# Optimization experiments

Measured on AMD Instinct MI355X. Metric: run time of the kernel, lower is better.

Reference implementation:

```python
import jax, jax.numpy as jnp
import numpy as np

B, S, H = 2, 1024, 1024
NH, NKV, HD = 16, 4, 64
E, TOPK, I = 8, 2, 3584
EPS = 1e-5
THETA = 1e6


def setup_inputs() -> dict:
    key = jax.random.key(0)
    ks = jax.random.split(key, 12)
    def w(k, shape, fan_in):
        return jax.random.normal(k, shape, dtype=jnp.float32) * (1.0 / np.sqrt(fan_in))
    return {
        "hidden_states": jax.random.normal(ks[0], (B, S, H), dtype=jnp.float32),
        "position_ids": jnp.broadcast_to(jnp.arange(S, dtype=jnp.int64)[None, :], (B, S)),
        "ln1_w": jnp.ones((H,), jnp.float32),
        "ln2_w": jnp.ones((H,), jnp.float32),
        "wq": w(ks[1], (H, NH * HD), H),
        "wk": w(ks[2], (H, NKV * HD), H),
        "wv": w(ks[3], (H, NKV * HD), H),
        "wo": w(ks[4], (NH * HD, H), NH * HD),
        "router_w": w(ks[5], (H, E), H),
        "w_gate": w(ks[6], (E, H, I), H),
        "w_up": w(ks[7], (E, H, I), H),
        "w_down": w(ks[8], (E, I, H), I),
    }


def _rmsnorm(x, w):
    xf = x.astype(jnp.float32)
    return (xf * jax.lax.rsqrt(jnp.mean(xf * xf, -1, keepdims=True) + EPS)).astype(x.dtype) * w


def _rope(x, pos):
    # x: [B,S,nh,HD], pos: [B,S]
    inv_freq = 1.0 / (THETA ** (jnp.arange(0, HD, 2, dtype=jnp.float32) / HD))
    ang = pos.astype(jnp.float32)[..., None] * inv_freq            # [B,S,HD/2]
    emb = jnp.concatenate([ang, ang], axis=-1)                      # [B,S,HD]
    cos, sin = jnp.cos(emb)[:, :, None, :], jnp.sin(emb)[:, :, None, :]
    x1, x2 = x[..., : HD // 2], x[..., HD // 2:]
    rot = jnp.concatenate([-x2, x1], axis=-1)
    return x * cos + rot * sin


def _forward(hidden_states, position_ids, ln1_w, ln2_w, wq, wk, wv, wo,
             router_w, w_gate, w_up, w_down):
    residual = hidden_states
    x = _rmsnorm(hidden_states, ln1_w)

    # ---- attention (GQA, causal, RoPE) ----
    q = (x @ wq).reshape(B, S, NH, HD)
    k = (x @ wk).reshape(B, S, NKV, HD)
    v = (x @ wv).reshape(B, S, NKV, HD)
    q = _rope(q, position_ids)
    k = _rope(k, position_ids)
    rep = NH // NKV
    k = jnp.repeat(k, rep, axis=2)  # [B,S,NH,HD]
    v = jnp.repeat(v, rep, axis=2)
    scores = jnp.einsum("bqhd,bkhd->bhqk", q, k) / np.sqrt(HD)
    causal = jnp.tril(jnp.ones((S, S), bool))
    scores = jnp.where(causal[None, None], scores, jnp.finfo(scores.dtype).min)
    probs = jax.nn.softmax(scores, axis=-1)
    attn = jnp.einsum("bhqk,bkhd->bqhd", probs, v).reshape(B, S, NH * HD)
    hidden = residual + attn @ wo

    # ---- MoE MLP ----
    residual = hidden
    xn = _rmsnorm(hidden, ln2_w).reshape(-1, H)               # [T,H]
    T = xn.shape[0]
    logits = xn @ router_w                                    # [T,E]
    rprobs = jax.nn.softmax(logits.astype(jnp.float32), axis=-1)
    topv, topi = jax.lax.top_k(rprobs, TOPK)                  # [T,TOPK]
    topv = topv / jnp.sum(topv, axis=-1, keepdims=True)       # normalize_top_k_affinities
    weights = jnp.zeros((T, E), jnp.float32).at[jnp.arange(T)[:, None], topi].set(topv)
    g = jnp.einsum("th,ehi->eti", xn, w_gate)                 # [E,T,I]
    u = jnp.einsum("th,ehi->eti", xn, w_up)
    a = jax.nn.silu(g) * u
    eo = jnp.einsum("eti,eih->eth", a, w_down)                # [E,T,H]
    moe = jnp.einsum("eth,te->th", eo, weights).reshape(B, S, H)
    return residual + moe


def reference(hidden_states, position_ids, ln1_w, ln2_w, wq, wk, wv, wo,
              router_w, w_gate, w_up, w_down):
    return _forward(hidden_states, position_ids, ln1_w, ln2_w, wq, wk, wv, wo,
                    router_w, w_gate, w_up, w_down)
```

## Files before the change

kernel.cpp:

```cpp
#include <hip/hip_runtime.h>
#include <hip/hip_bf16.h>
#include <math.h>

#define Bc 2
#define Sc 1024
#define Hc 1024
#define NHc 16
#define NKVc 4
#define HDc 64
#define Ec 8
#define TOPKc 2
#define Ic 3584
#define Tc (Bc*Sc)
#define EPSc 1e-5f

typedef __attribute__((ext_vector_type(8))) short bf16x8;
typedef __attribute__((ext_vector_type(4))) float f32x4;

__device__ __forceinline__ unsigned short f2bf(float f) {
    union { float f; unsigned u; } v; v.f = f;
    unsigned r = v.u + 0x7fffu + ((v.u >> 16) & 1u);
    return (unsigned short)(r >> 16);
}

__device__ __forceinline__ unsigned cvt_pk_bf16(float lo, float hi) {
    unsigned r;
    asm("v_cvt_pk_bf16_f32 %0, %1, %2" : "=v"(r) : "v"(lo), "v"(hi));
    return r;
}

static const size_t OFF_XN1  = 0;
static const size_t OFF_QB   = 8*1024*1024;
static const size_t OFF_KB   = OFF_QB + 8*1024*1024;
static const size_t OFF_VB   = OFF_KB + 2*1024*1024;
static const size_t OFF_XN2F = OFF_VB + 2*1024*1024;
static const size_t OFF_XN2B = OFF_XN2F + 8*1024*1024;
static const size_t OFF_ACT  = OFF_XN2B + 4*1024*1024;
static const size_t OFF_ROUTE= OFF_ACT + (size_t)4096*3584*2;

__global__ __launch_bounds__(256) void rmsnorm_kernel(const float* __restrict__ x,
        const float* __restrict__ w, float* __restrict__ outf,
        unsigned short* __restrict__ outb) {
    int t = blockIdx.x;
    int tid = threadIdx.x;
    const float* row = x + (size_t)t * Hc;
    float ss = 0.f;
    for (int h = tid; h < Hc; h += 256) { float v = row[h]; ss += v*v; }
    __shared__ float red[256];
    red[tid] = ss; __syncthreads();
    for (int s = 128; s > 0; s >>= 1) { if (tid < s) red[tid] += red[tid+s]; __syncthreads(); }
    float scale = rsqrtf(red[0] / (float)Hc + EPSc);
    for (int h = tid; h < Hc; h += 256) {
        float v = row[h] * scale * w[h];
        outf[(size_t)t*Hc + h] = v;
        if (outb) outb[(size_t)t*Hc + h] = f2bf(v);
    }
}

__global__ __launch_bounds__(256) void qkv_gemm(const float* __restrict__ A,
        const float* __restrict__ wq, const float* __restrict__ wk, const float* __restrict__ wv,
        float* __restrict__ qout, float* __restrict__ kout, float* __restrict__ vout) {
    __shared__ float As[64][17];
    __shared__ float Bs[16][65];
    int n0 = blockIdx.x * 64;
    int m0 = blockIdx.y * 64;
    int tid = threadIdx.x;
    int tx = tid & 15, ty = tid >> 4;
    const float* Bp; int ldb, c0;
    if (n0 < 1024)      { Bp = wq; ldb = 1024; c0 = n0; }
    else if (n0 < 1280) { Bp = wk; ldb = 256;  c0 = n0 - 1024; }
    else                { Bp = wv; ldb = 256;  c0 = n0 - 1280; }
    float acc[4][4] = {};
    for (int k0 = 0; k0 < 1024; k0 += 16) {
        #pragma unroll
        for (int i = 0; i < 4; i++) {
            int lin = tid + i*256; int r = lin >> 4, k = lin & 15;
            As[r][k] = A[(size_t)(m0 + r)*Hc + k0 + k];
        }
        #pragma unroll
        for (int i = 0; i < 4; i++) {
            int lin = tid + i*256; int r = lin >> 6, c = lin & 63;
            Bs[r][c] = Bp[(size_t)(k0 + r)*ldb + c0 + c];
        }
        __syncthreads();
        #pragma unroll
        for (int kk = 0; kk < 16; kk++) {
            float a[4], b[4];
            #pragma unroll
            for (int i = 0; i < 4; i++) a[i] = As[ty*4+i][kk];
            #pragma unroll
            for (int j = 0; j < 4; j++) b[j] = Bs[kk][tx*4+j];
            #pragma unroll
            for (int i = 0; i < 4; i++)
                #pragma unroll
                for (int j = 0; j < 4; j++) acc[i][j] += a[i]*b[j];
        }
        __syncthreads();
    }
    #pragma unroll
    for (int i = 0; i < 4; i++) {
        int m = m0 + ty*4 + i;
        #pragma unroll
        for (int j = 0; j < 4; j++) {
            int n = n0 + tx*4 + j;
            float val = acc[i][j];
            if (n < 1024)      qout[(size_t)m*1024 + n] = val;
            else if (n < 1280) kout[(size_t)m*256 + (n-1024)] = val;
            else               vout[(size_t)m*256 + (n-1280)] = val;
        }
    }
}

__global__ __launch_bounds__(256) void rope_kernel(float* __restrict__ q, float* __restrict__ k) {
    int idx = blockIdx.x*256 + threadIdx.x;
    const int total = Tc*(NHc+NKVc)*32;
    if (idx >= total) return;
    int d = idx & 31;
    int rest = idx >> 5;
    int head = rest % (NHc+NKVc);
    int t = rest / (NHc+NKVc);
    int s = t & (Sc-1);
    float inv = exp2f(-(float)d * 0.62286152f);
    float ang = (float)s * inv;
    float c = cosf(ang), sn = sinf(ang);
    float* base;
    if (head < NHc) base = q + (size_t)t*1024 + head*64;
    else            base = k + (size_t)t*256  + (head-NHc)*64;
    float x1 = base[d], x2 = base[d+32];
    base[d]    = x1*c - x2*sn;
    base[d+32] = x2*c + x1*sn;
}

__global__ __launch_bounds__(256) void attn_kernel(const float* __restrict__ q,
        const float* __restrict__ kbuf, const float* __restrict__ vbuf,
        float* __restrict__ attn) {
    __shared__ float Qs[64][65];
    __shared__ float KVs[64][65];
    __shared__ float Ps[64][65];
    __shared__ float m_s[64], l_s[64], al_s[64];
    int q0 = blockIdx.x * 64;
    int h  = blockIdx.y;
    int b  = blockIdx.z;
    int hk = h >> 2;
    int tid = threadIdx.x;
    int tx = tid & 15, ty = tid >> 4;
    #pragma unroll
    for (int i = 0; i < 16; i++) {
        int lin = tid + i*256; int r = lin >> 6, d = lin & 63;
        Qs[r][d] = q[((size_t)(b*Sc + q0 + r))*1024 + h*64 + d];
    }
    if (tid < 64) { m_s[tid] = -INFINITY; l_s[tid] = 0.f; }
    float O[4][4] = {};
    for (int j0 = 0; j0 <= q0; j0 += 64) {
        __syncthreads();
        #pragma unroll
        for (int i = 0; i < 16; i++) {
            int lin = tid + i*256; int r = lin >> 6, d = lin & 63;
            KVs[r][d] = kbuf[((size_t)(b*Sc + j0 + r))*256 + hk*64 + d];
        }
        __syncthreads();
        float sc[4][4] = {};
        for (int d = 0; d < 64; d++) {
            float a[4], bb[4];
            #pragma unroll
            for (int i = 0; i < 4; i++) a[i] = Qs[ty*4+i][d];
            #pragma unroll
            for (int j = 0; j < 4; j++) bb[j] = KVs[tx*4+j][d];
            #pragma unroll
            for (int i = 0; i < 4; i++)
                #pragma unroll
                for (int j = 0; j < 4; j++) sc[i][j] += a[i]*bb[j];
        }
        bool diag = (j0 == q0);
        #pragma unroll
        for (int i = 0; i < 4; i++) {
            int r = ty*4+i;
            #pragma unroll
            for (int j = 0; j < 4; j++) {
                int c = tx*4+j;
                float v = sc[i][j]*0.125f;
                if (diag && c > r) v = -1e30f;
                Ps[r][c] = v;
            }
        }
        __syncthreads();
        if (tid < 64) {
            int r = tid;
            float mx = -1e30f;
            for (int c = 0; c < 64; c++) mx = fmaxf(mx, Ps[r][c]);
            float newm = fmaxf(m_s[r], mx);
            float alpha = expf(m_s[r] - newm);
            float sum = 0.f;
            for (int c = 0; c < 64; c++) { float p = expf(Ps[r][c] - newm); Ps[r][c] = p; sum += p; }
            l_s[r] = l_s[r]*alpha + sum;
            m_s[r] = newm;
            al_s[r] = alpha;
        }
        #pragma unroll
        for (int i = 0; i < 16; i++) {
            int lin = tid + i*256; int r = lin >> 6, d = lin & 63;
            KVs[r][d] = vbuf[((size_t)(b*Sc + j0 + r))*256 + hk*64 + d];
        }
        __syncthreads();
        #pragma unroll
        for (int i = 0; i < 4; i++) {
            float al = al_s[ty*4+i];
            #pragma unroll
            for (int j = 0; j < 4; j++) O[i][j] *= al;
        }
        for (int c = 0; c < 64; c++) {
            float p[4], vv[4];
            #pragma unroll
            for (int i = 0; i < 4; i++) p[i] = Ps[ty*4+i][c];
            #pragma unroll
            for (int j = 0; j < 4; j++) vv[j] = KVs[c][tx*4+j];
            #pragma unroll
            for (int i = 0; i < 4; i++)
                #pragma unroll
                for (int j = 0; j < 4; j++) O[i][j] += p[i]*vv[j];
        }
    }
    #pragma unroll
    for (int i = 0; i < 4; i++) {
        int r = ty*4+i;
        float inv_l = 1.f / l_s[r];
        int m = b*Sc + q0 + r;
        #pragma unroll
        for (int j = 0; j < 4; j++) {
            int d = tx*4+j;
            attn[(size_t)m*1024 + h*64 + d] = O[i][j]*inv_l;
        }
    }
}

__global__ __launch_bounds__(256) void wo_gemm(const float* __restrict__ A,
        const float* __restrict__ wo, const float* __restrict__ resid,
        float* __restrict__ out) {
    __shared__ float As[64][17];
    __shared__ float Bs[16][65];
    int n0 = blockIdx.x * 64;
    int m0 = blockIdx.y * 64;
    int tid = threadIdx.x;
    int tx = tid & 15, ty = tid >> 4;
    float acc[4][4] = {};
    for (int k0 = 0; k0 < 1024; k0 += 16) {
        #pragma unroll
        for (int i = 0; i < 4; i++) {
            int lin = tid + i*256; int r = lin >> 4, k = lin & 15;
            As[r][k] = A[(size_t)(m0 + r)*Hc + k0 + k];
        }
        #pragma unroll
        for (int i = 0; i < 4; i++) {
            int lin = tid + i*256; int r = lin >> 6, c = lin & 63;
            Bs[r][c] = wo[(size_t)(k0 + r)*Hc + n0 + c];
        }
        __syncthreads();
        #pragma unroll
        for (int kk = 0; kk < 16; kk++) {
            float a[4], b[4];
            #pragma unroll
            for (int i = 0; i < 4; i++) a[i] = As[ty*4+i][kk];
            #pragma unroll
            for (int j = 0; j < 4; j++) b[j] = Bs[kk][tx*4+j];
            #pragma unroll
            for (int i = 0; i < 4; i++)
                #pragma unroll
                for (int j = 0; j < 4; j++) acc[i][j] += a[i]*b[j];
        }
        __syncthreads();
    }
    #pragma unroll
    for (int i = 0; i < 4; i++) {
        int m = m0 + ty*4 + i;
        #pragma unroll
        for (int j = 0; j < 4; j++) {
            int n = n0 + tx*4 + j;
            out[(size_t)m*Hc + n] = acc[i][j] + resid[(size_t)m*Hc + n];
        }
    }
}

__global__ __launch_bounds__(256) void router_kernel(const float* __restrict__ xn2,
        const float* __restrict__ rw, int* __restrict__ counts,
        int* __restrict__ topk_e, float* __restrict__ topk_w) {
    int t = blockIdx.x, tid = threadIdx.x;
    float part[8] = {};
    for (int h = tid; h < 1024; h += 256) {
        float x = xn2[(size_t)t*Hc + h];
        #pragma unroll
        for (int e = 0; e < 8; e++) part[e] += x * rw[h*8 + e];
    }
    __shared__ float red[8][256];
    #pragma unroll
    for (int e = 0; e < 8; e++) red[e][tid] = part[e];
    __syncthreads();
    for (int s = 128; s > 0; s >>= 1) {
        if (tid < s) {
            #pragma unroll
            for (int e = 0; e < 8; e++) red[e][tid] += red[e][tid+s];
        }
        __syncthreads();
    }
    if (tid == 0) {
        float lg[8]; float mx = -1e30f;
        for (int e = 0; e < 8; e++) { lg[e] = red[e][0]; mx = fmaxf(mx, lg[e]); }
        float p[8]; float sum = 0.f;
        for (int e = 0; e < 8; e++) { p[e] = expf(lg[e]-mx); sum += p[e]; }
        for (int e = 0; e < 8; e++) p[e] /= sum;
        int e0 = 0;
        for (int e = 1; e < 8; e++) if (p[e] > p[e0]) e0 = e;
        int e1 = -1;
        for (int e = 0; e < 8; e++) { if (e == e0) continue; if (e1 < 0 || p[e] > p[e1]) e1 = e; }
        float w0 = p[e0], w1 = p[e1]; float wsum = w0 + w1; w0 /= wsum; w1 /= wsum;
        topk_e[t*2] = e0; topk_e[t*2+1] = e1;
        topk_w[t*2] = w0; topk_w[t*2+1] = w1;
        atomicAdd(&counts[e0], 1); atomicAdd(&counts[e1], 1);
    }
}

__global__ void prefix_kernel(const int* __restrict__ counts, int* __restrict__ offsets) {
    if (threadIdx.x == 0 && blockIdx.x == 0) {
        int acc = 0;
        for (int e = 0; e < 8; e++) { offsets[e] = acc; acc += counts[e]; }
    }
}

__global__ __launch_bounds__(256) void fill_kernel(const int* __restrict__ topk_e,
        const float* __restrict__ topk_w, const int* __restrict__ offsets,
        int* __restrict__ fill, int* __restrict__ list_tok, float* __restrict__ list_w) {
    int t = blockIdx.x*256 + threadIdx.x;
    if (t >= Tc) return;
    #pragma unroll
    for (int j = 0; j < 2; j++) {
        int e = topk_e[t*2+j]; float w = topk_w[t*2+j];
        int slot = atomicAdd(&fill[e], 1);
        list_tok[offsets[e]+slot] = t;
        list_w[offsets[e]+slot] = w;
    }
}

__global__ __launch_bounds__(256) void gemm_gateup(const unsigned short* __restrict__ xn2b,
        const float* __restrict__ wg, const float* __restrict__ wu,
        const int* __restrict__ counts, const int* __restrict__ offsets,
        const int* __restrict__ list_tok, unsigned short* __restrict__ act) {
    int e = blockIdx.z;
    int cnt = counts[e];
    int m0 = blockIdx.y * 128;
    if (m0 >= cnt) return;
    int n0 = blockIdx.x * 64;
    int aoff = offsets[e];
    __shared__ unsigned short As[128*40];
    __shared__ unsigned short Bg[64*40];
    __shared__ unsigned short Bu[64*40];
    __shared__ int toks[128];
    int tid = threadIdx.x;
    if (tid < 128) toks[tid] = list_tok[aoff + min(m0 + tid, cnt-1)];
    __syncthreads();
    const float* Bgp = wg + (size_t)e*Hc*Ic + n0;
    const float* Bup = wu + (size_t)e*Hc*Ic + n0;
    int lane = tid & 63, wave = tid >> 6;
    int wm = wave >> 1, wn = wave & 1;
    int ml = lane & 15, quad = lane >> 4;
    int kp = tid & 15, n4 = tid >> 4;
    f32x4 accg[4][2] = {}, accu[4][2] = {};
    for (int k0 = 0; k0 < Hc; k0 += 32) {
        #pragma unroll
        for (int it = 0; it < 2; it++) {
            int lin = tid + it*256;
            int r = lin >> 2, part = lin & 3;
            uint4 v = *reinterpret_cast<const uint4*>(xn2b + (size_t)toks[r]*Hc + k0 + part*8);
            *reinterpret_cast<uint4*>(&As[r*40 + part*8]) = v;
        }
        {
            const float* gp = Bgp + (size_t)(k0 + 2*kp)*Ic + n4*4;
            const float* up = Bup + (size_t)(k0 + 2*kp)*Ic + n4*4;
            f32x4 g0 = *reinterpret_cast<const f32x4*>(gp);
            f32x4 g1 = *reinterpret_cast<const f32x4*>(gp + Ic);
            f32x4 u0 = *reinterpret_cast<const f32x4*>(up);
            f32x4 u1 = *reinterpret_cast<const f32x4*>(up + Ic);
            #pragma unroll
            for (int j = 0; j < 4; j++) {
                *reinterpret_cast<unsigned*>(&Bg[(n4*4+j)*40 + 2*kp]) = cvt_pk_bf16(g0[j], g1[j]);
                *reinterpret_cast<unsigned*>(&Bu[(n4*4+j)*40 + 2*kp]) = cvt_pk_bf16(u0[j], u1[j]);
            }
        }
        __syncthreads();
        bf16x8 a[4], bg[2], bu[2];
        #pragma unroll
        for (int mt = 0; mt < 4; mt++)
            a[mt] = *reinterpret_cast<const bf16x8*>(&As[(wm*64 + mt*16 + ml)*40 + quad*8]);
        #pragma unroll
        for (int nt = 0; nt < 2; nt++) {
            bg[nt] = *reinterpret_cast<const bf16x8*>(&Bg[(wn*32 + nt*16 + ml)*40 + quad*8]);
            bu[nt] = *reinterpret_cast<const bf16x8*>(&Bu[(wn*32 + nt*16 + ml)*40 + quad*8]);
        }
        #pragma unroll
        for (int mt = 0; mt < 4; mt++)
            #pragma unroll
            for (int nt = 0; nt < 2; nt++) {
                accg[mt][nt] = __builtin_amdgcn_mfma_f32_16x16x32_bf16(a[mt], bg[nt], accg[mt][nt], 0, 0, 0);
                accu[mt][nt] = __builtin_amdgcn_mfma_f32_16x16x32_bf16(a[mt], bu[nt], accu[mt][nt], 0, 0, 0);
            }
        __syncthreads();
    }
    #pragma unroll
    for (int mt = 0; mt < 4; mt++)
        #pragma unroll
        for (int nt = 0; nt < 2; nt++)
            #pragma unroll
            for (int rg = 0; rg < 4; rg++) {
                int rowl = wm*64 + mt*16 + quad*4 + rg;
                if (m0 + rowl < cnt) {
                    int n = n0 + wn*32 + nt*16 + ml;
                    float g = accg[mt][nt][rg], u = accu[mt][nt][rg];
                    float sg = g / (1.f + expf(-g));
                    act[(size_t)(aoff + m0 + rowl)*Ic + n] = f2bf(sg * u);
                }
            }
}

__global__ __launch_bounds__(256) void gemm_down(const unsigned short* __restrict__ act,
        const float* __restrict__ wd, const int* __restrict__ counts,
        const int* __restrict__ offsets, const int* __restrict__ list_tok,
        const float* __restrict__ list_w, float* __restrict__ out) {
    int e = blockIdx.z;
    int cnt = counts[e];
    int m0 = blockIdx.y * 128;
    if (m0 >= cnt) return;
    int n0 = blockIdx.x * 128;
    int aoff = offsets[e];
    __shared__ unsigned short As[128*40];
    __shared__ unsigned short Bs[128*40];
    const unsigned short* A = act + (size_t)(aoff + m0)*Ic;
    const float* B = wd + (size_t)e*Ic*Hc + n0;
    int rowclamp = cnt - 1 - m0;
    int tid = threadIdx.x;
    int lane = tid & 63, wave = tid >> 6;
    int wm = wave >> 1, wn = wave & 1;
    int ml = lane & 15, quad = lane >> 4;
    f32x4 acc[4][4] = {};
    for (int k0 = 0; k0 < Ic; k0 += 32) {
        #pragma unroll
        for (int it = 0; it < 2; it++) {
            int lin = tid + it*256;
            int r = lin >> 2, part = lin & 3;
            int rc = min(r, rowclamp);
            uint4 v = *reinterpret_cast<const uint4*>(A + (size_t)rc*Ic + k0 + part*8);
            *reinterpret_cast<uint4*>(&As[r*40 + part*8]) = v;
        }
        #pragma unroll
        for (int it = 0; it < 2; it++) {
            int lin = tid + it*256;
            int kp = lin & 15, n4 = lin >> 4;
            const float* bp = B + (size_t)(k0 + 2*kp)*Hc + n4*4;
            f32x4 b0 = *reinterpret_cast<const f32x4*>(bp);
            f32x4 b1 = *reinterpret_cast<const f32x4*>(bp + Hc);
            #pragma unroll
            for (int j = 0; j < 4; j++)
                *reinterpret_cast<unsigned*>(&Bs[(n4*4+j)*40 + 2*kp]) = cvt_pk_bf16(b0[j], b1[j]);
        }
        __syncthreads();
        bf16x8 a[4], b[4];
        #pragma unroll
        for (int mt = 0; mt < 4; mt++)
            a[mt] = *reinterpret_cast<const bf16x8*>(&As[(wm*64 + mt*16 + ml)*40 + quad*8]);
        #pragma unroll
        for (int nt = 0; nt < 4; nt++)
            b[nt] = *reinterpret_cast<const bf16x8*>(&Bs[(wn*64 + nt*16 + ml)*40 + quad*8]);
        #pragma unroll
        for (int mt = 0; mt < 4; mt++)
            #pragma unroll
            for (int nt = 0; nt < 4; nt++)
                acc[mt][nt] = __builtin_amdgcn_mfma_f32_16x16x32_bf16(a[mt], b[nt], acc[mt][nt], 0, 0, 0);
        __syncthreads();
    }
    #pragma unroll
    for (int mt = 0; mt < 4; mt++)
        #pragma unroll
        for (int nt = 0; nt < 4; nt++)
            #pragma unroll
            for (int rg = 0; rg < 4; rg++) {
                int rowl = wm*64 + mt*16 + quad*4 + rg;
                if (m0 + rowl < cnt) {
                    int t = list_tok[aoff + m0 + rowl];
                    float w = list_w[aoff + m0 + rowl];
                    int n = n0 + wn*64 + nt*16 + ml;
                    atomicAdd(&out[(size_t)t*Hc + n], w * acc[mt][nt][rg]);
                }
            }
}

extern "C" void kernel_launch(void* const* d_in, const int* in_sizes, int n_in,
                              void* d_out, int out_size, void* d_ws, size_t ws_size,
                              hipStream_t stream) {
    const float* hidden = (const float*)d_in[0];
    const float* ln1 = (const float*)d_in[2];
    const float* ln2 = (const float*)d_in[3];
    const float* wq  = (const float*)d_in[4];
    const float* wk  = (const float*)d_in[5];
    const float* wv  = (const float*)d_in[6];
    const float* wo  = (const float*)d_in[7];
    const float* rw  = (const float*)d_in[8];
    const float* wg  = (const float*)d_in[9];
    const float* wu  = (const float*)d_in[10];
    const float* wd  = (const float*)d_in[11];
    float* out = (float*)d_out;
    char* ws = (char*)d_ws;

    float* xn1f  = (float*)(ws + OFF_XN1);
    float* attnf = xn1f;
    float* qb    = (float*)(ws + OFF_QB);
    float* kb    = (float*)(ws + OFF_KB);
    float* vb    = (float*)(ws + OFF_VB);
    float* xn2f  = (float*)(ws + OFF_XN2F);
    unsigned short* xn2b = (unsigned short*)(ws + OFF_XN2B);
    unsigned short* act  = (unsigned short*)(ws + OFF_ACT);
    int*   route    = (int*)(ws + OFF_ROUTE);
    int*   counts   = route;
    int*   fillc    = route + 8;
    int*   offsets  = route + 16;
    int*   topk_e   = route + 24;
    float* topk_w   = (float*)(route + 24 + 2*Tc);
    int*   list_tok = route + 24 + 4*Tc;
    float* list_w   = (float*)(route + 24 + 6*Tc);

    hipMemsetAsync(counts, 0, 16*sizeof(int), stream);

    rmsnorm_kernel<<<Tc, 256, 0, stream>>>(hidden, ln1, xn1f, nullptr);
    qkv_gemm<<<dim3(24, 32), 256, 0, stream>>>(xn1f, wq, wk, wv, qb, kb, vb);
    rope_kernel<<<(Tc*(NHc+NKVc)*32 + 255)/256, 256, 0, stream>>>(qb, kb);
    attn_kernel<<<dim3(16, 16, 2), 256, 0, stream>>>(qb, kb, vb, attnf);
    wo_gemm<<<dim3(16, 32), 256, 0, stream>>>(attnf, wo, hidden, out);
    rmsnorm_kernel<<<Tc, 256, 0, stream>>>(out, ln2, xn2f, xn2b);
    router_kernel<<<Tc, 256, 0, stream>>>(xn2f, rw, counts, topk_e, topk_w);
    prefix_kernel<<<1, 64, 0, stream>>>(counts, offsets);
    fill_kernel<<<(Tc+255)/256, 256, 0, stream>>>(topk_e, topk_w, offsets, fillc, list_tok, list_w);
    gemm_gateup<<<dim3(56, 16, 8), 256, 0, stream>>>(xn2b, wg, wu, counts, offsets, list_tok, act);
    gemm_down<<<dim3(8, 16, 8), 256, 0, stream>>>(act, wd, counts, offsets, list_tok, list_w, out);
}
```

Baseline: 1.244 ms.

## Register-prefetch next K tile in MoE GEMMs and halve down-proj M tile

Both MoE GEMM kernels now load the next K slice of activations and fp32 weights into registers while the current slice runs through MFMA, which hides global-load latency behind compute. The gate/up kernel also changes its thread-to-(k,n) mapping for the weight loads. The down-projection kernel drops from a 128-row to a 64-row M tile and doubles grid.y, giving more blocks per expert. The costs are higher register pressure, and in the down kernel each block now re-reads its weight tile for fewer rows.

```diff
diff --git a/kernel.cpp b/kernel.cpp
--- a/kernel.cpp
+++ b/kernel.cpp
@@ -361,30 +361,35 @@
     int lane = tid & 63, wave = tid >> 6;
     int wm = wave >> 1, wn = wave & 1;
     int ml = lane & 15, quad = lane >> 4;
-    int kp = tid & 15, n4 = tid >> 4;
+    int n4 = tid & 15, kp = tid >> 4;
+    int ar0 = tid >> 2, ap0 = tid & 3;
+    int ar1 = (tid + 256) >> 2, ap1 = (tid + 256) & 3;
+
+    uint4 pa0, pa1;
+    f32x4 pg0, pg1, pu0, pu1;
+    #define GU_LOAD(K0) { \
+        pa0 = *reinterpret_cast<const uint4*>(xn2b + (size_t)toks[ar0]*Hc + (K0) + ap0*8); \
+        pa1 = *reinterpret_cast<const uint4*>(xn2b + (size_t)toks[ar1]*Hc + (K0) + ap1*8); \
+        const float* gp = Bgp + (size_t)((K0) + 2*kp)*Ic + n4*4; \
+        const float* up = Bup + (size_t)((K0) + 2*kp)*Ic + n4*4; \
+        pg0 = *reinterpret_cast<const f32x4*>(gp); \
+        pg1 = *reinterpret_cast<const f32x4*>(gp + Ic); \
+        pu0 = *reinterpret_cast<const f32x4*>(up); \
+        pu1 = *reinterpret_cast<const f32x4*>(up + Ic); \
+    }
+
     f32x4 accg[4][2] = {}, accu[4][2] = {};
+    GU_LOAD(0);
     for (int k0 = 0; k0 < Hc; k0 += 32) {
-        #pragma unroll
-        for (int it = 0; it < 2; it++) {
-            int lin = tid + it*256;
-            int r = lin >> 2, part = lin & 3;
-            uint4 v = *reinterpret_cast<const uint4*>(xn2b + (size_t)toks[r]*Hc + k0 + part*8);
-            *reinterpret_cast<uint4*>(&As[r*40 + part*8]) = v;
-        }
-        {
-            const float* gp = Bgp + (size_t)(k0 + 2*kp)*Ic + n4*4;
-            const float* up = Bup + (size_t)(k0 + 2*kp)*Ic + n4*4;
-            f32x4 g0 = *reinterpret_cast<const f32x4*>(gp);
-            f32x4 g1 = *reinterpret_cast<const f32x4*>(gp + Ic);
-            f32x4 u0 = *reinterpret_cast<const f32x4*>(up);
-            f32x4 u1 = *reinterpret_cast<const f32x4*>(up + Ic);
-            #pragma unroll
-            for (int j = 0; j < 4; j++) {
-                *reinterpret_cast<unsigned*>(&Bg[(n4*4+j)*40 + 2*kp]) = cvt_pk_bf16(g0[j], g1[j]);
-                *reinterpret_cast<unsigned*>(&Bu[(n4*4+j)*40 + 2*kp]) = cvt_pk_bf16(u0[j], u1[j]);
-            }
-        }
-        __syncthreads();
+        *reinterpret_cast<uint4*>(&As[ar0*40 + ap0*8]) = pa0;
+        *reinterpret_cast<uint4*>(&As[ar1*40 + ap1*8]) = pa1;
+        #pragma unroll
+        for (int j = 0; j < 4; j++) {
+            *reinterpret_cast<unsigned*>(&Bg[(n4*4+j)*40 + 2*kp]) = cvt_pk_bf16(pg0[j], pg1[j]);
+            *reinterpret_cast<unsigned*>(&Bu[(n4*4+j)*40 + 2*kp]) = cvt_pk_bf16(pu0[j], pu1[j]);
+        }
+        __syncthreads();
+        if (k0 + 32 < Hc) GU_LOAD(k0 + 32);
         bf16x8 a[4], bg[2], bu[2];
         #pragma unroll
         for (int mt = 0; mt < 4; mt++)
@@ -403,6 +408,7 @@
             }
         __syncthreads();
     }
+    #undef GU_LOAD
     #pragma unroll
     for (int mt = 0; mt < 4; mt++)
         #pragma unroll
@@ -425,11 +431,11 @@
         const float* __restrict__ list_w, float* __restrict__ out) {
     int e = blockIdx.z;
     int cnt = counts[e];
-    int m0 = blockIdx.y * 128;
+    int m0 = blockIdx.y * 64;
     if (m0 >= cnt) return;
     int n0 = blockIdx.x * 128;
     int aoff = offsets[e];
-    __shared__ unsigned short As[128*40];
+    __shared__ unsigned short As[64*40];
     __shared__ unsigned short Bs[128*40];
     const unsigned short* A = act + (size_t)(aoff + m0)*Ic;
     const float* B = wd + (size_t)e*Ic*Hc + n0;
@@ -438,49 +444,56 @@
     int lane = tid & 63, wave = tid >> 6;
     int wm = wave >> 1, wn = wave & 1;
     int ml = lane & 15, quad = lane >> 4;
-    f32x4 acc[4][4] = {};
+    int ar = tid >> 2, ap = tid & 3;
+    int arc = min(ar, rowclamp);
+    int n4a = tid & 31, kpa = tid >> 5;
+    int n4b = n4a, kpb = kpa + 8;
+
+    uint4 pa;
+    f32x4 pb0a, pb1a, pb0b, pb1b;
+    #define DN_LOAD(K0) { \
+        pa = *reinterpret_cast<const uint4*>(A + (size_t)arc*Ic + (K0) + ap*8); \
+        const float* bpa = B + (size_t)((K0) + 2*kpa)*Hc + n4a*4; \
+        const float* bpb = B + (size_t)((K0) + 2*kpb)*Hc + n4b*4; \
+        pb0a = *reinterpret_cast<const f32x4*>(bpa); \
+        pb1a = *reinterpret_cast<const f32x4*>(bpa + Hc); \
+        pb0b = *reinterpret_cast<const f32x4*>(bpb); \
+        pb1b = *reinterpret_cast<const f32x4*>(bpb + Hc); \
+    }
+
+    f32x4 acc[2][4] = {};
+    DN_LOAD(0);
     for (int k0 = 0; k0 < Ic; k0 += 32) {
-        #pragma unroll
-        for (int it = 0; it < 2; it++) {
-            int lin = tid + it*256;
-            int r = lin >> 2, part = lin & 3;
-            int rc = min(r, rowclamp);
-            uint4 v = *reinterpret_cast<const uint4*>(A + (size_t)rc*Ic + k0 + part*8);
-            *reinterpret_cast<uint4*>(&As[r*40 + part*8]) = v;
-        }
-        #pragma unroll
-        for (int it = 0; it < 2; it++) {
-            int lin = tid + it*256;
-            int kp = lin & 15, n4 = lin >> 4;
-            const float* bp = B + (size_t)(k0 + 2*kp)*Hc + n4*4;
-            f32x4 b0 = *reinterpret_cast<const f32x4*>(bp);
-            f32x4 b1 = *reinterpret_cast<const f32x4*>(bp + Hc);
-            #pragma unroll
-            for (int j = 0; j < 4; j++)
-                *reinterpret_cast<unsigned*>(&Bs[(n4*4+j)*40 + 2*kp]) = cvt_pk_bf16(b0[j], b1[j]);
-        }
-        __syncthreads();
-        bf16x8 a[4], b[4];
-        #pragma unroll
-        for (int mt = 0; mt < 4; mt++)
-            a[mt] = *reinterpret_cast<const bf16x8*>(&As[(wm*64 + mt*16 + ml)*40 + quad*8]);
+        *reinterpret_cast<uint4*>(&As[ar*40 + ap*8]) = pa;
+        #pragma unroll
+        for (int j = 0; j < 4; j++) {
+            *reinterpret_cast<unsigned*>(&Bs[(n4a*4+j)*40 + 2*kpa]) = cvt_pk_bf16(pb0a[j], pb1a[j]);
+            *reinterpret_cast<unsigned*>(&Bs[(n4b*4+j)*40 + 2*kpb]) = cvt_pk_bf16(pb0b[j], pb1b[j]);
+        }
+        __syncthreads();
+        if (k0 + 32 < Ic) DN_LOAD(k0 + 32);
+        bf16x8 a[2], b[4];
+        #pragma unroll
+        for (int mt = 0; mt < 2; mt++)
+            a[mt] = *reinterpret_cast<const bf16x8*>(&As[(wm*32 + mt*16 + ml)*40 + quad*8]);
         #pragma unroll
         for (int nt = 0; nt < 4; nt++)
             b[nt] = *reinterpret_cast<const bf16x8*>(&Bs[(wn*64 + nt*16 + ml)*40 + quad*8]);
         #pragma unroll
-        for (int mt = 0; mt < 4; mt++)
+        for (int mt = 0; mt < 2; mt++)
             #pragma unroll
             for (int nt = 0; nt < 4; nt++)
                 acc[mt][nt] = __builtin_amdgcn_mfma_f32_16x16x32_bf16(a[mt], b[nt], acc[mt][nt], 0, 0, 0);
         __syncthreads();
     }
-    #pragma unroll
-    for (int mt = 0; mt < 4; mt++)
+    #undef DN_LOAD
+    #pragma unroll
+    for (int mt = 0; mt < 2; mt++)
         #pragma unroll
         for (int nt = 0; nt < 4; nt++)
             #pragma unroll
             for (int rg = 0; rg < 4; rg++) {
-                int rowl = wm*64 + mt*16 + quad*4 + rg;
+                int rowl = wm*32 + mt*16 + quad*4 + rg;
                 if (m0 + rowl < cnt) {
                     int t = list_tok[aoff + m0 + rowl];
                     float w = list_w[aoff + m0 + rowl];
@@ -536,5 +549,5 @@
     prefix_kernel<<<1, 64, 0, stream>>>(counts, offsets);
     fill_kernel<<<(Tc+255)/256, 256, 0, stream>>>(topk_e, topk_w, offsets, fillc, list_tok, list_w);
     gemm_gateup<<<dim3(56, 16, 8), 256, 0, stream>>>(xn2b, wg, wu, counts, offsets, list_tok, act);
-    gemm_down<<<dim3(8, 16, 8), 256, 0, stream>>>(act, wd, counts, offsets, list_tok, list_w, out);
-}
+    gemm_down<<<dim3(8, 32, 8), 256, 0, stream>>>(act, wd, counts, offsets, list_tok, list_w, out);
+}
```

New measurement: 1.307 ms. 1.05x slower.

## Double-buffer MoE GEMMs with direct global-to-LDS loads and narrower down tiles

Applied to the files above, without the earlier changes.

Both MoE expert GEMMs now issue direct global-to-LDS loads (global_load_lds) into double-buffered shared tiles. The next K-slice is prefetched while the current one is computed, replacing register-staged loads and the sync before compute. FP32 weights now stay in LDS as fp32 and are converted to bf16 when fragments are read. The down GEMM halves its N tile to 64, doubling the grid. The aims are to overlap memory traffic with MFMA work and raise occupancy, at the cost of more LDS per block, conversion work repeated across waves, possible LDS bank conflicts on strided reads, and re-reading the activation tile for each of the twice-as-many down blocks.

```diff
diff --git a/kernel.cpp b/kernel.cpp
--- a/kernel.cpp
+++ b/kernel.cpp
@@ -28,6 +28,10 @@
     asm("v_cvt_pk_bf16_f32 %0, %1, %2" : "=v"(r) : "v"(lo), "v"(hi));
     return r;
 }
+
+#define GLL(g, l) __builtin_amdgcn_global_load_lds( \
+    (const __attribute__((address_space(1))) void*)(g), \
+    (__attribute__((address_space(3))) void*)(l), 16, 0, 0)
 
 static const size_t OFF_XN1  = 0;
 static const size_t OFF_QB   = 8*1024*1024;
@@ -349,9 +353,9 @@
     if (m0 >= cnt) return;
     int n0 = blockIdx.x * 64;
     int aoff = offsets[e];
-    __shared__ unsigned short As[128*40];
-    __shared__ unsigned short Bg[64*40];
-    __shared__ unsigned short Bu[64*40];
+    __shared__ alignas(16) unsigned short As[2][128*32];
+    __shared__ alignas(16) float Bgs[2][32*64];
+    __shared__ alignas(16) float Bus[2][32*64];
     __shared__ int toks[128];
     int tid = threadIdx.x;
     if (tid < 128) toks[tid] = list_tok[aoff + min(m0 + tid, cnt-1)];
@@ -361,38 +365,50 @@
     int lane = tid & 63, wave = tid >> 6;
     int wm = wave >> 1, wn = wave & 1;
     int ml = lane & 15, quad = lane >> 4;
-    int kp = tid & 15, n4 = tid >> 4;
+    int wb = wave * 64;
+
+    const unsigned short* aS0 = xn2b + (size_t)toks[tid>>2]*Hc + (tid&3)*8;
+    const unsigned short* aS1 = xn2b + (size_t)toks[(tid+256)>>2]*Hc + (tid&3)*8;
+    const float* gS0 = Bgp + (size_t)(tid>>4)*Ic + (tid&15)*4;
+    const float* gS1 = Bgp + (size_t)((tid>>4)+16)*Ic + (tid&15)*4;
+    const float* uS0 = Bup + (size_t)(tid>>4)*Ic + (tid&15)*4;
+    const float* uS1 = Bup + (size_t)((tid>>4)+16)*Ic + (tid&15)*4;
+
+    #define GU_STAGE(buf, K0) do { \
+        GLL(aS0 + (K0), &As[buf][wb*8]); \
+        GLL(aS1 + (K0), &As[buf][(256+wb)*8]); \
+        GLL(gS0 + (size_t)(K0)*Ic, &Bgs[buf][wb*4]); \
+        GLL(gS1 + (size_t)(K0)*Ic, &Bgs[buf][(256+wb)*4]); \
+        GLL(uS0 + (size_t)(K0)*Ic, &Bus[buf][wb*4]); \
+        GLL(uS1 + (size_t)(K0)*Ic, &Bus[buf][(256+wb)*4]); \
+    } while(0)
+
     f32x4 accg[4][2] = {}, accu[4][2] = {};
-    for (int k0 = 0; k0 < Hc; k0 += 32) {
-        #pragma unroll
-        for (int it = 0; it < 2; it++) {
-            int lin = tid + it*256;
-            int r = lin >> 2, part = lin & 3;
-            uint4 v = *reinterpret_cast<const uint4*>(xn2b + (size_t)toks[r]*Hc + k0 + part*8);
-            *reinterpret_cast<uint4*>(&As[r*40 + part*8]) = v;
-        }
-        {
-            const float* gp = Bgp + (size_t)(k0 + 2*kp)*Ic + n4*4;
-            const float* up = Bup + (size_t)(k0 + 2*kp)*Ic + n4*4;
-            f32x4 g0 = *reinterpret_cast<const f32x4*>(gp);
-            f32x4 g1 = *reinterpret_cast<const f32x4*>(gp + Ic);
-            f32x4 u0 = *reinterpret_cast<const f32x4*>(up);
-            f32x4 u1 = *reinterpret_cast<const f32x4*>(up + Ic);
+    GU_STAGE(0, 0);
+    asm volatile("s_waitcnt vmcnt(0)" ::: "memory");
+    __syncthreads();
+    int cur = 0;
+    for (int ks = 0; ks < Hc/32; ks++) {
+        if (ks + 1 < Hc/32) GU_STAGE(cur^1, (ks+1)*32);
+        bf16x8 a[4];
+        #pragma unroll
+        for (int mt = 0; mt < 4; mt++) {
+            int R = wm*64 + mt*16 + ml;
+            a[mt] = *reinterpret_cast<const bf16x8*>(&As[cur][R*32 + quad*8]);
+        }
+        bf16x8 bg[2], bu[2];
+        #pragma unroll
+        for (int nt = 0; nt < 2; nt++) {
+            int n = wn*32 + nt*16 + ml;
+            const float* pg = &Bgs[cur][quad*512 + n];
+            const float* pu = &Bus[cur][quad*512 + n];
+            union { bf16x8 v; unsigned u[4]; } tg, tu;
             #pragma unroll
             for (int j = 0; j < 4; j++) {
-                *reinterpret_cast<unsigned*>(&Bg[(n4*4+j)*40 + 2*kp]) = cvt_pk_bf16(g0[j], g1[j]);
-                *reinterpret_cast<unsigned*>(&Bu[(n4*4+j)*40 + 2*kp]) = cvt_pk_bf16(u0[j], u1[j]);
+                tg.u[j] = cvt_pk_bf16(pg[(2*j)*64], pg[(2*j+1)*64]);
+                tu.u[j] = cvt_pk_bf16(pu[(2*j)*64], pu[(2*j+1)*64]);
             }
-        }
-        __syncthreads();
-        bf16x8 a[4], bg[2], bu[2];
-        #pragma unroll
-        for (int mt = 0; mt < 4; mt++)
-            a[mt] = *reinterpret_cast<const bf16x8*>(&As[(wm*64 + mt*16 + ml)*40 + quad*8]);
-        #pragma unroll
-        for (int nt = 0; nt < 2; nt++) {
-            bg[nt] = *reinterpret_cast<const bf16x8*>(&Bg[(wn*32 + nt*16 + ml)*40 + quad*8]);
-            bu[nt] = *reinterpret_cast<const bf16x8*>(&Bu[(wn*32 + nt*16 + ml)*40 + quad*8]);
+            bg[nt] = tg.v; bu[nt] = tu.v;
         }
         #pragma unroll
         for (int mt = 0; mt < 4; mt++)
@@ -401,8 +417,11 @@
                 accg[mt][nt] = __builtin_amdgcn_mfma_f32_16x16x32_bf16(a[mt], bg[nt], accg[mt][nt], 0, 0, 0);
                 accu[mt][nt] = __builtin_amdgcn_mfma_f32_16x16x32_bf16(a[mt], bu[nt], accu[mt][nt], 0, 0, 0);
             }
-        __syncthreads();
-    }
+        asm volatile("s_waitcnt vmcnt(0)" ::: "memory");
+        __syncthreads();
+        cur ^= 1;
+    }
+    #undef GU_STAGE
     #pragma unroll
     for (int mt = 0; mt < 4; mt++)
         #pragma unroll
@@ -427,64 +446,78 @@
     int cnt = counts[e];
     int m0 = blockIdx.y * 128;
     if (m0 >= cnt) return;
-    int n0 = blockIdx.x * 128;
+    int n0 = blockIdx.x * 64;
     int aoff = offsets[e];
-    __shared__ unsigned short As[128*40];
-    __shared__ unsigned short Bs[128*40];
-    const unsigned short* A = act + (size_t)(aoff + m0)*Ic;
-    const float* B = wd + (size_t)e*Ic*Hc + n0;
+    __shared__ alignas(16) unsigned short As[2][128*32];
+    __shared__ alignas(16) float Bs[2][32*64];
+    const unsigned short* Aexp = act + (size_t)(aoff + m0)*Ic;
+    const float* Bp = wd + (size_t)e*Ic*Hc + n0;
     int rowclamp = cnt - 1 - m0;
     int tid = threadIdx.x;
     int lane = tid & 63, wave = tid >> 6;
     int wm = wave >> 1, wn = wave & 1;
     int ml = lane & 15, quad = lane >> 4;
-    f32x4 acc[4][4] = {};
-    for (int k0 = 0; k0 < Ic; k0 += 32) {
-        #pragma unroll
-        for (int it = 0; it < 2; it++) {
-            int lin = tid + it*256;
-            int r = lin >> 2, part = lin & 3;
-            int rc = min(r, rowclamp);
-            uint4 v = *reinterpret_cast<const uint4*>(A + (size_t)rc*Ic + k0 + part*8);
-            *reinterpret_cast<uint4*>(&As[r*40 + part*8]) = v;
-        }
-        #pragma unroll
-        for (int it = 0; it < 2; it++) {
-            int lin = tid + it*256;
-            int kp = lin & 15, n4 = lin >> 4;
-            const float* bp = B + (size_t)(k0 + 2*kp)*Hc + n4*4;
-            f32x4 b0 = *reinterpret_cast<const f32x4*>(bp);
-            f32x4 b1 = *reinterpret_cast<const f32x4*>(bp + Hc);
+    int wb = wave * 64;
+
+    int R0 = min(tid >> 2, rowclamp);
+    int R1 = min((tid + 256) >> 2, rowclamp);
+    const unsigned short* aS0 = Aexp + (size_t)R0*Ic + (tid&3)*8;
+    const unsigned short* aS1 = Aexp + (size_t)R1*Ic + (tid&3)*8;
+    const float* bS0 = Bp + (size_t)(tid>>4)*Hc + (tid&15)*4;
+    const float* bS1 = Bp + (size_t)((tid>>4)+16)*Hc + (tid&15)*4;
+
+    #define DN_STAGE(buf, K0) do { \
+        GLL(aS0 + (K0), &As[buf][wb*8]); \
+        GLL(aS1 + (K0), &As[buf][(256+wb)*8]); \
+        GLL(bS0 + (size_t)(K0)*Hc, &Bs[buf][wb*4]); \
+        GLL(bS1 + (size_t)(K0)*Hc, &Bs[buf][(256+wb)*4]); \
+    } while(0)
+
+    f32x4 acc[4][2] = {};
+    DN_STAGE(0, 0);
+    asm volatile("s_waitcnt vmcnt(0)" ::: "memory");
+    __syncthreads();
+    int cur = 0;
+    for (int ks = 0; ks < Ic/32; ks++) {
+        if (ks + 1 < Ic/32) DN_STAGE(cur^1, (ks+1)*32);
+        bf16x8 a[4];
+        #pragma unroll
+        for (int mt = 0; mt < 4; mt++) {
+            int R = wm*64 + mt*16 + ml;
+            a[mt] = *reinterpret_cast<const bf16x8*>(&As[cur][R*32 + quad*8]);
+        }
+        bf16x8 b[2];
+        #pragma unroll
+        for (int nt = 0; nt < 2; nt++) {
+            int n = wn*32 + nt*16 + ml;
+            const float* pb = &Bs[cur][quad*512 + n];
+            union { bf16x8 v; unsigned u[4]; } tb;
             #pragma unroll
             for (int j = 0; j < 4; j++)
-                *reinterpret_cast<unsigned*>(&Bs[(n4*4+j)*40 + 2*kp]) = cvt_pk_bf16(b0[j], b1[j]);
-        }
-        __syncthreads();
-        bf16x8 a[4], b[4];
+                tb.u[j] = cvt_pk_bf16(pb[(2*j)*64], pb[(2*j+1)*64]);
+            b[nt] = tb.v;
+        }
         #pragma unroll
         for (int mt = 0; mt < 4; mt++)
-            a[mt] = *reinterpret_cast<const bf16x8*>(&As[(wm*64 + mt*16 + ml)*40 + quad*8]);
-        #pragma unroll
-        for (int nt = 0; nt < 4; nt++)
-            b[nt] = *reinterpret_cast<const bf16x8*>(&Bs[(wn*64 + nt*16 + ml)*40 + quad*8]);
-        #pragma unroll
-        for (int mt = 0; mt < 4; mt++)
-            #pragma unroll
-            for (int nt = 0; nt < 4; nt++)
+            #pragma unroll
+            for (int nt = 0; nt < 2; nt++)
                 acc[mt][nt] = __builtin_amdgcn_mfma_f32_16x16x32_bf16(a[mt], b[nt], acc[mt][nt], 0, 0, 0);
-        __syncthreads();
-    }
+        asm volatile("s_waitcnt vmcnt(0)" ::: "memory");
+        __syncthreads();
+        cur ^= 1;
+    }
+    #undef DN_STAGE
     #pragma unroll
     for (int mt = 0; mt < 4; mt++)
         #pragma unroll
-        for (int nt = 0; nt < 4; nt++)
+        for (int nt = 0; nt < 2; nt++)
             #pragma unroll
             for (int rg = 0; rg < 4; rg++) {
                 int rowl = wm*64 + mt*16 + quad*4 + rg;
                 if (m0 + rowl < cnt) {
                     int t = list_tok[aoff + m0 + rowl];
                     float w = list_w[aoff + m0 + rowl];
-                    int n = n0 + wn*64 + nt*16 + ml;
+                    int n = n0 + wn*32 + nt*16 + ml;
                     atomicAdd(&out[(size_t)t*Hc + n], w * acc[mt][nt][rg]);
                 }
             }
@@ -536,5 +569,5 @@
     prefix_kernel<<<1, 64, 0, stream>>>(counts, offsets);
     fill_kernel<<<(Tc+255)/256, 256, 0, stream>>>(topk_e, topk_w, offsets, fillc, list_tok, list_w);
     gemm_gateup<<<dim3(56, 16, 8), 256, 0, stream>>>(xn2b, wg, wu, counts, offsets, list_tok, act);
-    gemm_down<<<dim3(8, 16, 8), 256, 0, stream>>>(act, wd, counts, offsets, list_tok, list_w, out);
-}
+    gemm_down<<<dim3(16, 16, 8), 256, 0, stream>>>(act, wd, counts, offsets, list_tok, list_w, out);
+}
```

Result: faster. 1.154 ms (-7.2%).
